# Performance work log

Measured on AMD Instinct MI355X. Metric: run time of the kernel, lower is better.

Reference implementation:

```python
import jax, jax.numpy as jnp
import numpy as np

FEATURE_DIM = 128
HIDDEN_DIM = 64
MAPPING_SIZE = 64
SCALE = 10.0
B, N, H, W = 8, 65536, 56, 56


def setup_inputs() -> dict:
    key = jax.random.key(0)
    ks = jax.random.split(key, 12)
    features = jax.random.normal(ks[0], (B, FEATURE_DIM, H, W), dtype=jnp.float32)
    # points in [-1, 1]^3
    points = jax.random.uniform(ks[1], (B, N, 3), dtype=jnp.float32, minval=-1.0, maxval=1.0)
    # realistic pinhole intrinsics for a 56x56 feature map
    k_mat = jnp.array([[56.0, 0.0, 28.0], [0.0, 56.0, 28.0], [0.0, 0.0, 1.0]], dtype=jnp.float32)
    k = jnp.broadcast_to(k_mat, (B, 3, 3))
    # extrinsics: identity rotation, translate z by 2 so points are in front of camera
    rt_mat = jnp.concatenate([jnp.eye(3, dtype=jnp.float32), jnp.array([[0.0], [0.0], [2.0]], dtype=jnp.float32)], axis=1)
    rt = jnp.broadcast_to(rt_mat, (B, 3, 4))
    # learned params
    B_gauss = jax.random.normal(ks[2], (MAPPING_SIZE, 3), dtype=jnp.float32) * SCALE
    input_dim = FEATURE_DIM + 2 * MAPPING_SIZE
    W1 = jax.random.normal(ks[3], (input_dim, HIDDEN_DIM), dtype=jnp.float32) * 0.05
    b1 = jnp.zeros((HIDDEN_DIM,), dtype=jnp.float32)
    W2 = jax.random.normal(ks[4], (HIDDEN_DIM, HIDDEN_DIM), dtype=jnp.float32) * 0.05
    b2 = jnp.zeros((HIDDEN_DIM,), dtype=jnp.float32)
    W3 = jax.random.normal(ks[5], (HIDDEN_DIM, HIDDEN_DIM), dtype=jnp.float32) * 0.05
    b3 = jnp.zeros((HIDDEN_DIM,), dtype=jnp.float32)
    W4 = jax.random.normal(ks[6], (HIDDEN_DIM, 1), dtype=jnp.float32) * 0.05
    b4 = jnp.zeros((1,), dtype=jnp.float32)
    return {"features": features, "points": points, "k": k, "rt": rt,
            "B_gauss": B_gauss, "W1": W1, "b1": b1, "W2": W2, "b2": b2,
            "W3": W3, "b3": b3, "W4": W4, "b4": b4}


def _grid_sample_bilinear_zeros(grid, x, y):
    # grid: (B, C, H, W); x, y: (B, N) pixel coords (align_corners=False already unnormalized)
    Bc, C, Hc, Wc = grid.shape
    g = jnp.transpose(grid, (0, 2, 3, 1))  # (B, H, W, C)
    x0 = jnp.floor(x)
    y0 = jnp.floor(y)
    wx1 = x - x0  # frac
    wy1 = y - y0
    wx0 = 1.0 - wx1
    wy0 = 1.0 - wy1
    x0i = x0.astype(jnp.int32)
    y0i = y0.astype(jnp.int32)
    bidx = jnp.arange(Bc, dtype=jnp.int32)[:, None]  # (B, 1)

    def gather(ix, iy):
        inb = ((ix >= 0) & (ix < Wc) & (iy >= 0) & (iy < Hc)).astype(grid.dtype)  # (B, N)
        vals = g[bidx, jnp.clip(iy, 0, Hc - 1), jnp.clip(ix, 0, Wc - 1)]  # (B, N, C)
        return vals * inb[..., None]

    out = (gather(x0i, y0i) * (wx0 * wy0)[..., None]
           + gather(x0i + 1, y0i) * (wx1 * wy0)[..., None]
           + gather(x0i, y0i + 1) * (wx0 * wy1)[..., None]
           + gather(x0i + 1, y0i + 1) * (wx1 * wy1)[..., None])
    return out  # (B, N, C)


def reference(features, points, k, rt, B_gauss, W1, b1, W2, b2, W3, b3, W4, b4):
    Bc, Nc, _ = points.shape
    Hc, Wc = features.shape[-2:]
    # --- camera projection ---
    homo = jnp.concatenate([points, jnp.ones((Bc, Nc, 1), dtype=points.dtype)], axis=2)  # (B,N,4)
    cam = jnp.einsum('bij,bnj->bni', rt, homo)   # (B,N,3)
    img = jnp.einsum('bij,bnj->bni', k, cam)     # (B,N,3)
    z = img[:, :, 2:3] + 1e-8
    uv = img[:, :, :2] / z
    valid = (img[:, :, 2:3] > 0).astype(points.dtype)  # (B,N,1)
    u_norm = (2.0 * uv[..., 0] + 1.0) / Wc - 1.0
    v_norm = (2.0 * uv[..., 1] + 1.0) / Hc - 1.0
    # grid_sample align_corners=False unnormalization: ix = ((g+1)*W - 1)/2
    x = ((u_norm + 1.0) * Wc - 1.0) * 0.5
    y = ((v_norm + 1.0) * Hc - 1.0) * 0.5
    img_feats = _grid_sample_bilinear_zeros(features, x, y) * valid  # (B,N,C)
    # --- Fourier mapping ---
    x_proj = (2.0 * np.pi) * jnp.einsum('bnd,md->bnm', points, B_gauss)  # (B,N,M)
    coord_feats = jnp.concatenate([jnp.sin(x_proj), jnp.cos(x_proj)], axis=-1)  # (B,N,2M)
    # --- MLP ---
    inp = jnp.concatenate([img_feats, coord_feats], axis=2)  # (B,N,C+2M)
    h = jax.nn.relu(inp @ W1 + b1)
    h = jax.nn.relu(h @ W2 + b2)
    h = jax.nn.relu(h @ W3 + b3)
    out = h @ W4 + b4  # (B,N,1)
    return out
```

## Files before the change

kernel.cpp:

```cpp
#include <hip/hip_runtime.h>

#define FDIM 128
#define HDIM 64
#define MSIZE 64
#define IMG_W 56
#define IMG_H 56
#define NPIX (IMG_W * IMG_H)
#define NB 8
#define NPTS 65536

typedef _Float16 f16x8 __attribute__((ext_vector_type(8)));
typedef __fp16 hf16x2 __attribute__((ext_vector_type(2)));
typedef float f32x4 __attribute__((ext_vector_type(4)));

#define W2_OFF 16384
#define W3_OFF 20480
#define BG_OFF 49152
#define FT_BYTE_OFF 50176
#define TR16_BLOCKS (NPIX / 16 * NB)

__device__ __forceinline__ void lds_fence() {
    __asm__ volatile("s_waitcnt lgkmcnt(0)" ::: "memory");
}

__global__ __launch_bounds__(256) void prep_kernel(const float* __restrict__ in,
                                                   const float* __restrict__ W1,
                                                   const float* __restrict__ W2,
                                                   const float* __restrict__ W3,
                                                   const float* __restrict__ Bg,
                                                   _Float16* __restrict__ ws) {
    if (blockIdx.x < TR16_BLOCKS) {
        __shared__ float tile[16][133];
        _Float16* out = ws + FT_BYTE_OFF / 2;
        const int b = blockIdx.x / (NPIX / 16);
        const int pbase = (blockIdx.x % (NPIX / 16)) * 16;
        const int t = threadIdx.x;
        const float* src = in + (size_t)b * FDIM * NPIX;
        _Float16*    dst = out + (size_t)b * NPIX * FDIM;
        const int pq = t & 3;
        const int ch = t >> 2;
#pragma unroll
        for (int it = 0; it < 2; ++it) {
            const int c = it * 64 + ch;
            const float4 v = *(const float4*)(src + (size_t)c * NPIX + pbase + pq * 4);
            tile[pq * 4 + 0][c] = v.x;
            tile[pq * 4 + 1][c] = v.y;
            tile[pq * 4 + 2][c] = v.z;
            tile[pq * 4 + 3][c] = v.w;
        }
        __syncthreads();
        const int px = t >> 4;
        const int hk = (t & 15) * 8;
        union { f16x8 v; hf16x2 h[4]; } hv;
#pragma unroll
        for (int j = 0; j < 4; ++j)
            hv.h[j] = __builtin_amdgcn_cvt_pkrtz(tile[px][hk + 2 * j], tile[px][hk + 2 * j + 1]);
        *(f16x8*)(dst + (size_t)(pbase + px) * FDIM + hk) = hv.v;
    } else if (blockIdx.x < TR16_BLOCKS + 12) {
        const int t = (blockIdx.x - TR16_BLOCKS) * 256 + threadIdx.x;
        const int l = t & 63;
        const int q = l >> 4;
        const int col = l & 15;
        const int frag = t >> 6;
        if (frag < 32) {
            const int kt = frag >> 2, nt = frag & 3;
#pragma unroll
            for (int j = 0; j < 8; ++j) {
                int k = kt * 32 + q * 8 + j;
                int row = (k < 128) ? k : (128 + (k & 1) * 64 + ((k - 128) >> 1));
                ws[((size_t)(frag * 64 + l)) * 8 + j] = (_Float16)W1[row * HDIM + nt * 16 + col];
            }
        } else if (frag < 40) {
            const int f2 = frag - 32;
            const int kt = f2 >> 2, nt = f2 & 3;
#pragma unroll
            for (int j = 0; j < 8; ++j) {
                int row = kt * 32 + q * 8 + j;
                ws[W2_OFF + ((size_t)(f2 * 64 + l)) * 8 + j] = (_Float16)W2[row * HDIM + nt * 16 + col];
            }
        } else {
            const int f3 = frag - 40;
            const int kt = f3 >> 2, nt = f3 & 3;
#pragma unroll
            for (int j = 0; j < 8; ++j) {
                int row = kt * 32 + q * 8 + j;
                ws[W3_OFF + ((size_t)(f3 * 64 + l)) * 8 + j] = (_Float16)W3[row * HDIM + nt * 16 + col];
            }
        }
    } else {
        const int t = threadIdx.x;
        if (t < MSIZE) {
            float* bgs = (float*)((char*)ws + BG_OFF);
            bgs[t]       = Bg[t * 3 + 0];
            bgs[64 + t]  = Bg[t * 3 + 1];
            bgs[128 + t] = Bg[t * 3 + 2];
        }
    }
}

__global__ __launch_bounds__(256, 3) void decoder_mfma5(
    const _Float16* __restrict__ ft,
    const float* __restrict__ points,
    const float* __restrict__ Kmat, const float* __restrict__ Rt,
    const _Float16* __restrict__ wfrag,
    const float* __restrict__ b1, const float* __restrict__ b2,
    const float* __restrict__ b3,
    const float* __restrict__ W4, const float* __restrict__ b4,
    float* __restrict__ out) {
    __shared__ _Float16 w1l[16384];
    __shared__ _Float16 lds[4 * 32 * 72];
    const int tid = threadIdx.x;
    const int wid = tid >> 6;
    const int l   = tid & 63;
    const int q   = l >> 4;
    const int col = l & 15;
    const int b    = blockIdx.x & 7;
    const int grp  = blockIdx.x >> 3;
    const int base = b * NPTS + grp * 128 + wid * 32;
    _Float16* Ah = lds + wid * 32 * 72;
    const float* bgs = (const float*)((const char*)wfrag + BG_OFF);

#pragma unroll
    for (int i = 0; i < 8; ++i)
        ((f16x8*)w1l)[i * 256 + tid] = ((const f16x8*)wfrag)[i * 256 + tid];

    const int gid = base + (l & 31);
    const float px = points[(size_t)gid * 3 + 0];
    const float py = points[(size_t)gid * 3 + 1];
    const float pz = points[(size_t)gid * 3 + 2];
    const float* rt = Rt + b * 12;
    const float* km = Kmat + b * 9;
    float cx = rt[0] * px + rt[1] * py + rt[2]  * pz + rt[3];
    float cy = rt[4] * px + rt[5] * py + rt[6]  * pz + rt[7];
    float cz = rt[8] * px + rt[9] * py + rt[10] * pz + rt[11];
    float ix = km[0] * cx + km[1] * cy + km[2] * cz;
    float iy = km[3] * cx + km[4] * cy + km[5] * cz;
    float iz = km[6] * cx + km[7] * cy + km[8] * cz;
    float z  = iz + 1e-8f;
    float u  = ix / z;
    float v  = iy / z;
    float valid = (iz > 0.0f) ? 1.0f : 0.0f;
    float u_norm = (2.0f * u + 1.0f) / (float)IMG_W - 1.0f;
    float v_norm = (2.0f * v + 1.0f) / (float)IMG_H - 1.0f;
    float x = ((u_norm + 1.0f) * (float)IMG_W - 1.0f) * 0.5f;
    float y = ((v_norm + 1.0f) * (float)IMG_H - 1.0f) * 0.5f;
    float x0f = floorf(x), y0f = floorf(y);
    float wx1 = x - x0f, wy1 = y - y0f;
    float wx0 = 1.0f - wx1, wy0 = 1.0f - wy1;
    int x0 = (int)x0f, y0 = (int)y0f;
    int x1 = x0 + 1, y1 = y0 + 1;
    int x0c = x0 < 0 ? 0 : (x0 > IMG_W - 1 ? IMG_W - 1 : x0);
    int x1c = x1 < 0 ? 0 : (x1 > IMG_W - 1 ? IMG_W - 1 : x1);
    int y0c = y0 < 0 ? 0 : (y0 > IMG_H - 1 ? IMG_H - 1 : y0);
    int y1c = y1 < 0 ? 0 : (y1 > IMG_H - 1 ? IMG_H - 1 : y1);
    float mx0 = (x0 >= 0 && x0 < IMG_W) ? 1.0f : 0.0f;
    float mx1 = (x1 >= 0 && x1 < IMG_W) ? 1.0f : 0.0f;
    float my0 = (y0 >= 0 && y0 < IMG_H) ? 1.0f : 0.0f;
    float my1 = (y1 >= 0 && y1 < IMG_H) ? 1.0f : 0.0f;
    const int pb = b * NPIX;
    float r_w00 = wx0 * wy0 * mx0 * my0 * valid;
    float r_w10 = wx1 * wy0 * mx1 * my0 * valid;
    float r_w01 = wx0 * wy1 * mx0 * my1 * valid;
    float r_w11 = wx1 * wy1 * mx1 * my1 * valid;
    int r_i00 = (pb + y0c * IMG_W + x0c) * FDIM;
    int r_i10 = (pb + y0c * IMG_W + x1c) * FDIM;
    int r_i01 = (pb + y1c * IMG_W + x0c) * FDIM;
    int r_i11 = (pb + y1c * IMG_W + x1c) * FDIM;

    float wv0[2], wv1[2], wv2[2], wv3[2];
    int   iv0[2], iv1[2], iv2[2], iv3[2];
    float qx[2], qy[2], qz[2];
#pragma unroll
    for (int mt = 0; mt < 2; ++mt) {
        const int src = mt * 16 + col;
        wv0[mt] = __shfl(r_w00, src);
        wv1[mt] = __shfl(r_w10, src);
        wv2[mt] = __shfl(r_w01, src);
        wv3[mt] = __shfl(r_w11, src);
        iv0[mt] = __shfl(r_i00, src);
        iv1[mt] = __shfl(r_i10, src);
        iv2[mt] = __shfl(r_i01, src);
        iv3[mt] = __shfl(r_i11, src);
        qx[mt]  = __shfl(px, src);
        qy[mt]  = __shfl(py, src);
        qz[mt]  = __shfl(pz, src);
    }

    __syncthreads();

    const f32x4 zero4 = {0.0f, 0.0f, 0.0f, 0.0f};
    f32x4 acc[2][4];
#pragma unroll
    for (int mt = 0; mt < 2; ++mt)
#pragma unroll
        for (int nt = 0; nt < 4; ++nt) acc[mt][nt] = zero4;

    const int co0 = q * 8;
    f16x8 a00 = *(const f16x8*)(ft + iv0[0] + co0);
    f16x8 a10 = *(const f16x8*)(ft + iv1[0] + co0);
    f16x8 a01 = *(const f16x8*)(ft + iv2[0] + co0);
    f16x8 a11 = *(const f16x8*)(ft + iv3[0] + co0);
    const int co1 = 32 + q * 8;
    f16x8 e00 = *(const f16x8*)(ft + iv0[0] + co1);
    f16x8 e10 = *(const f16x8*)(ft + iv1[0] + co1);
    f16x8 e01 = *(const f16x8*)(ft + iv2[0] + co1);
    f16x8 e11 = *(const f16x8*)(ft + iv3[0] + co1);

#pragma unroll
    for (int ktf = 0; ktf < 4; ++ktf) {
        const f32x4 bgx = *(const f32x4*)(bgs + ktf * 16 + q * 4);
        const f32x4 bgy = *(const f32x4*)(bgs + 64 + ktf * 16 + q * 4);
        const f32x4 bgz = *(const f32x4*)(bgs + 128 + ktf * 16 + q * 4);
        f16x8 bf[4];
#pragma unroll
        for (int nt = 0; nt < 4; ++nt)
            bf[nt] = *(const f16x8*)(w1l + ((size_t)(((4 + ktf) * 4 + nt) * 64 + l)) * 8);
#pragma unroll
        for (int mt = 0; mt < 2; ++mt) {
            union { f16x8 v; hf16x2 h[4]; } af;
#pragma unroll
            for (int i = 0; i < 4; ++i) {
                float t = bgx[i] * qx[mt] + bgy[i] * qy[mt] + bgz[i] * qz[mt];
                float tf = __builtin_amdgcn_fractf(t);
                af.h[i] = __builtin_amdgcn_cvt_pkrtz(__builtin_amdgcn_sinf(tf),
                                                     __builtin_amdgcn_cosf(tf));
            }
#pragma unroll
            for (int nt = 0; nt < 4; ++nt)
                acc[mt][nt] = __builtin_amdgcn_mfma_f32_16x16x32_f16(af.v, bf[nt], acc[mt][nt], 0, 0, 0);
        }
    }

    _Float16 wh[2][4];
#pragma unroll
    for (int mt = 0; mt < 2; ++mt) {
        wh[mt][0] = (_Float16)wv0[mt]; wh[mt][1] = (_Float16)wv1[mt];
        wh[mt][2] = (_Float16)wv2[mt]; wh[mt][3] = (_Float16)wv3[mt];
    }
#pragma unroll
    for (int s = 0; s < 8; ++s) {
        const int mt = s >> 2;
        f16x8 t00, t10, t01, t11;
        if (s < 6) {
            const int nmt = (s + 2) >> 2, nktg = (s + 2) & 3;
            const int co = nktg * 32 + q * 8;
            t00 = *(const f16x8*)(ft + iv0[nmt] + co);
            t10 = *(const f16x8*)(ft + iv1[nmt] + co);
            t01 = *(const f16x8*)(ft + iv2[nmt] + co);
            t11 = *(const f16x8*)(ft + iv3[nmt] + co);
        }
        f16x8 af = a00 * wh[mt][0] + a10 * wh[mt][1] + a01 * wh[mt][2] + a11 * wh[mt][3];
        const int ktg = s & 3;
#pragma unroll
        for (int nt = 0; nt < 4; ++nt) {
            f16x8 bf = *(const f16x8*)(w1l + ((size_t)((ktg * 4 + nt) * 64 + l)) * 8);
            acc[mt][nt] = __builtin_amdgcn_mfma_f32_16x16x32_f16(af, bf, acc[mt][nt], 0, 0, 0);
        }
        a00 = e00; a10 = e10; a01 = e01; a11 = e11;
        e00 = t00; e10 = t10; e01 = t01; e11 = t11;
    }

    f16x8 bfW[8];
#pragma unroll
    for (int f = 0; f < 8; ++f)
        bfW[f] = *(const f16x8*)(wfrag + W2_OFF + ((size_t)(f * 64 + l)) * 8);

    float bb[4];
#pragma unroll
    for (int nt = 0; nt < 4; ++nt) bb[nt] = b1[nt * 16 + col];
#pragma unroll
    for (int mt = 0; mt < 2; ++mt)
#pragma unroll
        for (int nt = 0; nt < 4; ++nt)
#pragma unroll
            for (int r = 0; r < 4; ++r) {
                float hv = fmaxf(acc[mt][nt][r] + bb[nt], 0.0f);
                Ah[(mt * 16 + q * 4 + r) * 72 + nt * 16 + col] = (_Float16)hv;
            }
    lds_fence();

#pragma unroll
    for (int mt = 0; mt < 2; ++mt)
#pragma unroll
        for (int nt = 0; nt < 4; ++nt) acc[mt][nt] = zero4;
#pragma unroll
    for (int ktl = 0; ktl < 2; ++ktl)
#pragma unroll
        for (int mt = 0; mt < 2; ++mt) {
            f16x8 af = *(const f16x8*)(&Ah[(mt * 16 + col) * 72 + ktl * 32 + q * 8]);
#pragma unroll
            for (int nt = 0; nt < 4; ++nt)
                acc[mt][nt] = __builtin_amdgcn_mfma_f32_16x16x32_f16(af, bfW[ktl * 4 + nt], acc[mt][nt], 0, 0, 0);
        }

#pragma unroll
    for (int f = 0; f < 8; ++f)
        bfW[f] = *(const f16x8*)(wfrag + W3_OFF + ((size_t)(f * 64 + l)) * 8);

    lds_fence();
#pragma unroll
    for (int nt = 0; nt < 4; ++nt) bb[nt] = b2[nt * 16 + col];
#pragma unroll
    for (int mt = 0; mt < 2; ++mt)
#pragma unroll
        for (int nt = 0; nt < 4; ++nt)
#pragma unroll
            for (int r = 0; r < 4; ++r) {
                float hv = fmaxf(acc[mt][nt][r] + bb[nt], 0.0f);
                Ah[(mt * 16 + q * 4 + r) * 72 + nt * 16 + col] = (_Float16)hv;
            }
    lds_fence();

#pragma unroll
    for (int mt = 0; mt < 2; ++mt)
#pragma unroll
        for (int nt = 0; nt < 4; ++nt) acc[mt][nt] = zero4;
#pragma unroll
    for (int ktl = 0; ktl < 2; ++ktl)
#pragma unroll
        for (int mt = 0; mt < 2; ++mt) {
            f16x8 af = *(const f16x8*)(&Ah[(mt * 16 + col) * 72 + ktl * 32 + q * 8]);
#pragma unroll
            for (int nt = 0; nt < 4; ++nt)
                acc[mt][nt] = __builtin_amdgcn_mfma_f32_16x16x32_f16(af, bfW[ktl * 4 + nt], acc[mt][nt], 0, 0, 0);
        }

    float b3v[4], w4v[4];
#pragma unroll
    for (int nt = 0; nt < 4; ++nt) {
        b3v[nt] = b3[nt * 16 + col];
        w4v[nt] = W4[nt * 16 + col];
    }
    const float b4v = b4[0];
#pragma unroll
    for (int mt = 0; mt < 2; ++mt)
#pragma unroll
        for (int r = 0; r < 4; ++r) {
            float p = 0.0f;
#pragma unroll
            for (int nt = 0; nt < 4; ++nt)
                p = fmaf(fmaxf(acc[mt][nt][r] + b3v[nt], 0.0f), w4v[nt], p);
            p += __shfl_xor(p, 1);
            p += __shfl_xor(p, 2);
            p += __shfl_xor(p, 4);
            p += __shfl_xor(p, 8);
            if (col == 0) out[base + mt * 16 + q * 4 + r] = p + b4v;
        }
}

__global__ __launch_bounds__(64, 2) void decoder_valu(
    const float* __restrict__ feats, const float* __restrict__ points,
    const float* __restrict__ Kmat, const float* __restrict__ Rt,
    const float* __restrict__ Bg,
    const float* __restrict__ W1, const float* __restrict__ b1,
    const float* __restrict__ W2, const float* __restrict__ b2,
    const float* __restrict__ W3, const float* __restrict__ b3,
    const float* __restrict__ W4, const float* __restrict__ b4,
    float* __restrict__ out) {
    __shared__ float hbuf[64 * 65];
    const int tid = threadIdx.x;
    const int b   = blockIdx.x / (NPTS / 64);
    const int gid = blockIdx.x * 64 + tid;
    const float px = points[(size_t)gid * 3 + 0];
    const float py = points[(size_t)gid * 3 + 1];
    const float pz = points[(size_t)gid * 3 + 2];
    const float* rt = Rt + b * 12;
    const float* km = Kmat + b * 9;
    float cx = rt[0] * px + rt[1] * py + rt[2]  * pz + rt[3];
    float cy = rt[4] * px + rt[5] * py + rt[6]  * pz + rt[7];
    float cz = rt[8] * px + rt[9] * py + rt[10] * pz + rt[11];
    float ix = km[0] * cx + km[1] * cy + km[2] * cz;
    float iy = km[3] * cx + km[4] * cy + km[5] * cz;
    float iz = km[6] * cx + km[7] * cy + km[8] * cz;
    float z  = iz + 1e-8f;
    float u  = ix / z, v = iy / z;
    float valid = (iz > 0.0f) ? 1.0f : 0.0f;
    float u_norm = (2.0f * u + 1.0f) / (float)IMG_W - 1.0f;
    float v_norm = (2.0f * v + 1.0f) / (float)IMG_H - 1.0f;
    float x = ((u_norm + 1.0f) * (float)IMG_W - 1.0f) * 0.5f;
    float y = ((v_norm + 1.0f) * (float)IMG_H - 1.0f) * 0.5f;
    float x0f = floorf(x), y0f = floorf(y);
    float wx1 = x - x0f, wy1 = y - y0f;
    float wx0 = 1.0f - wx1, wy0 = 1.0f - wy1;
    int x0 = (int)x0f, y0 = (int)y0f;
    int x1 = x0 + 1, y1 = y0 + 1;
    int x0c = x0 < 0 ? 0 : (x0 > IMG_W - 1 ? IMG_W - 1 : x0);
    int x1c = x1 < 0 ? 0 : (x1 > IMG_W - 1 ? IMG_W - 1 : x1);
    int y0c = y0 < 0 ? 0 : (y0 > IMG_H - 1 ? IMG_H - 1 : y0);
    int y1c = y1 < 0 ? 0 : (y1 > IMG_H - 1 ? IMG_H - 1 : y1);
    float mx0 = (x0 >= 0 && x0 < IMG_W) ? 1.0f : 0.0f;
    float mx1 = (x1 >= 0 && x1 < IMG_W) ? 1.0f : 0.0f;
    float my0 = (y0 >= 0 && y0 < IMG_H) ? 1.0f : 0.0f;
    float my1 = (y1 >= 0 && y1 < IMG_H) ? 1.0f : 0.0f;
    float w00 = wx0 * wy0 * mx0 * my0 * valid;
    float w10 = wx1 * wy0 * mx1 * my0 * valid;
    float w01 = wx0 * wy1 * mx0 * my1 * valid;
    float w11 = wx1 * wy1 * mx1 * my1 * valid;
    float h[HDIM];
#pragma unroll
    for (int j = 0; j < HDIM; ++j) h[j] = b1[j];
    const float* fb = feats + (size_t)b * FDIM * NPIX;
    const int p00 = y0c * IMG_W + x0c, p10 = y0c * IMG_W + x1c;
    const int p01 = y1c * IMG_W + x0c, p11 = y1c * IMG_W + x1c;
#pragma unroll 1
    for (int c = 0; c < FDIM; ++c) {
        const float* fp = fb + (size_t)c * NPIX;
        float fv = w00 * fp[p00] + w10 * fp[p10] + w01 * fp[p01] + w11 * fp[p11];
        const float* wr = W1 + (size_t)c * HDIM;
#pragma unroll
        for (int j = 0; j < HDIM; ++j) h[j] = fmaf(fv, wr[j], h[j]);
    }
#pragma unroll 1
    for (int m = 0; m < MSIZE; ++m) {
        float t = Bg[m * 3 + 0] * px + Bg[m * 3 + 1] * py + Bg[m * 3 + 2] * pz;
        float tf = t - floorf(t);
        float s = __builtin_amdgcn_sinf(tf);
        float c = __builtin_amdgcn_cosf(tf);
        const float* wsn = W1 + (size_t)(FDIM + m) * HDIM;
        const float* wcs = W1 + (size_t)(FDIM + MSIZE + m) * HDIM;
#pragma unroll
        for (int j = 0; j < HDIM; ++j)
            h[j] = fmaf(s, wsn[j], fmaf(c, wcs[j], h[j]));
    }
    float* myh = &hbuf[tid * 65];
#pragma unroll
    for (int j = 0; j < HDIM; ++j) myh[j] = fmaxf(h[j], 0.0f);
    float h2[HDIM];
#pragma unroll
    for (int j = 0; j < HDIM; ++j) h2[j] = b2[j];
#pragma unroll 1
    for (int i = 0; i < HDIM; ++i) {
        float hi = myh[i];
        const float* wr = W2 + (size_t)i * HDIM;
#pragma unroll
        for (int j = 0; j < HDIM; ++j) h2[j] = fmaf(hi, wr[j], h2[j]);
    }
#pragma unroll
    for (int j = 0; j < HDIM; ++j) myh[j] = fmaxf(h2[j], 0.0f);
#pragma unroll
    for (int j = 0; j < HDIM; ++j) h[j] = b3[j];
#pragma unroll 1
    for (int i = 0; i < HDIM; ++i) {
        float hi = myh[i];
        const float* wr = W3 + (size_t)i * HDIM;
#pragma unroll
        for (int j = 0; j < HDIM; ++j) h[j] = fmaf(hi, wr[j], h[j]);
    }
    float acc = b4[0];
#pragma unroll
    for (int j = 0; j < HDIM; ++j) acc = fmaf(fmaxf(h[j], 0.0f), W4[j], acc);
    out[gid] = acc;
}

extern "C" void kernel_launch(void* const* d_in, const int* in_sizes, int n_in,
                              void* d_out, int out_size, void* d_ws, size_t ws_size,
                              hipStream_t stream) {
    const float* feats = (const float*)d_in[0];
    const float* pts   = (const float*)d_in[1];
    const float* k     = (const float*)d_in[2];
    const float* rt    = (const float*)d_in[3];
    const float* Bg    = (const float*)d_in[4];
    const float* W1    = (const float*)d_in[5];
    const float* b1    = (const float*)d_in[6];
    const float* W2    = (const float*)d_in[7];
    const float* b2    = (const float*)d_in[8];
    const float* W3    = (const float*)d_in[9];
    const float* b3    = (const float*)d_in[10];
    const float* W4    = (const float*)d_in[11];
    const float* b4    = (const float*)d_in[12];
    float* out = (float*)d_out;

    const size_t ftBytes = (size_t)NB * NPIX * FDIM * sizeof(_Float16);

    if (ws_size >= FT_BYTE_OFF + ftBytes) {
        _Float16* wf = (_Float16*)d_ws;
        _Float16* ft = (_Float16*)((char*)d_ws + FT_BYTE_OFF);
        prep_kernel<<<TR16_BLOCKS + 13, 256, 0, stream>>>(feats, W1, W2, W3, Bg, wf);
        decoder_mfma5<<<NB * NPTS / 128, 256, 0, stream>>>(ft, pts, k, rt, wf,
                                                           b1, b2, b3, W4, b4, out);
    } else {
        decoder_valu<<<NB * NPTS / 64, 64, 0, stream>>>(feats, pts, k, rt, Bg,
                                                        W1, b1, W2, b2, W3, b3, W4, b4, out);
    }
}
```

Baseline: 174.0 us.

## Process two 32-point tiles per wave and prefetch second tile's gathers during MLP tail

Each wave now handles 64 points, split into two 32-point tiles that run one after the other, and the grid shrinks to half as many blocks. All 64 lanes now do the projection math, where before only 32 lanes did useful work. The second tile's feature gathers are issued before the first tile's MLP tail runs, so their latency can overlap that compute. It also halves how often each block copies W1 into LDS. The risks are higher register pressure from the second prefetch set, and fewer blocks for latency hiding.

Result: slower. 181.6 us (+4.4%).

```diff
diff --git a/kernel.cpp b/kernel.cpp
--- a/kernel.cpp
+++ b/kernel.cpp
@@ -98,7 +98,194 @@
     }
 }
 
-__global__ __launch_bounds__(256, 3) void decoder_mfma5(
+struct Rec {
+    float w0[2], w1[2], w2[2], w3[2];
+    int   i0[2], i1[2], i2[2], i3[2];
+    float qx[2], qy[2], qz[2];
+};
+struct Pref {
+    f16x8 a00, a10, a01, a11;
+    f16x8 e00, e10, e01, e11;
+};
+
+__device__ __forceinline__ Pref pre_issue(const _Float16* __restrict__ ft,
+                                          const Rec& R, int q) {
+    Pref P;
+    const int co0 = q * 8;
+    P.a00 = *(const f16x8*)(ft + R.i0[0] + co0);
+    P.a10 = *(const f16x8*)(ft + R.i1[0] + co0);
+    P.a01 = *(const f16x8*)(ft + R.i2[0] + co0);
+    P.a11 = *(const f16x8*)(ft + R.i3[0] + co0);
+    const int co1 = 32 + q * 8;
+    P.e00 = *(const f16x8*)(ft + R.i0[0] + co1);
+    P.e10 = *(const f16x8*)(ft + R.i1[0] + co1);
+    P.e01 = *(const f16x8*)(ft + R.i2[0] + co1);
+    P.e11 = *(const f16x8*)(ft + R.i3[0] + co1);
+    return P;
+}
+
+__device__ __forceinline__ void phaseF(f32x4 acc[2][4], const _Float16* __restrict__ w1l,
+                                       const float* __restrict__ bgs, const Rec& R,
+                                       int q, int l) {
+#pragma unroll
+    for (int ktf = 0; ktf < 4; ++ktf) {
+        const f32x4 bgx = *(const f32x4*)(bgs + ktf * 16 + q * 4);
+        const f32x4 bgy = *(const f32x4*)(bgs + 64 + ktf * 16 + q * 4);
+        const f32x4 bgz = *(const f32x4*)(bgs + 128 + ktf * 16 + q * 4);
+        f16x8 bf[4];
+#pragma unroll
+        for (int nt = 0; nt < 4; ++nt)
+            bf[nt] = *(const f16x8*)(w1l + ((size_t)(((4 + ktf) * 4 + nt) * 64 + l)) * 8);
+#pragma unroll
+        for (int mt = 0; mt < 2; ++mt) {
+            union { f16x8 v; hf16x2 h[4]; } af;
+#pragma unroll
+            for (int i = 0; i < 4; ++i) {
+                float t = bgx[i] * R.qx[mt] + bgy[i] * R.qy[mt] + bgz[i] * R.qz[mt];
+                float tf = __builtin_amdgcn_fractf(t);
+                af.h[i] = __builtin_amdgcn_cvt_pkrtz(__builtin_amdgcn_sinf(tf),
+                                                     __builtin_amdgcn_cosf(tf));
+            }
+#pragma unroll
+            for (int nt = 0; nt < 4; ++nt)
+                acc[mt][nt] = __builtin_amdgcn_mfma_f32_16x16x32_f16(af.v, bf[nt], acc[mt][nt], 0, 0, 0);
+        }
+    }
+}
+
+__device__ __forceinline__ void phaseI(f32x4 acc[2][4], const _Float16* __restrict__ ft,
+                                       const _Float16* __restrict__ w1l, const Rec& R,
+                                       Pref& P, int q, int l) {
+    _Float16 wh[2][4];
+#pragma unroll
+    for (int mt = 0; mt < 2; ++mt) {
+        wh[mt][0] = (_Float16)R.w0[mt]; wh[mt][1] = (_Float16)R.w1[mt];
+        wh[mt][2] = (_Float16)R.w2[mt]; wh[mt][3] = (_Float16)R.w3[mt];
+    }
+#pragma unroll
+    for (int s = 0; s < 8; ++s) {
+        const int mt = s >> 2;
+        f16x8 t00, t10, t01, t11;
+        if (s < 6) {
+            const int nmt = (s + 2) >> 2, nktg = (s + 2) & 3;
+            const int co = nktg * 32 + q * 8;
+            t00 = *(const f16x8*)(ft + R.i0[nmt] + co);
+            t10 = *(const f16x8*)(ft + R.i1[nmt] + co);
+            t01 = *(const f16x8*)(ft + R.i2[nmt] + co);
+            t11 = *(const f16x8*)(ft + R.i3[nmt] + co);
+        }
+        f16x8 af = P.a00 * wh[mt][0] + P.a10 * wh[mt][1] + P.a01 * wh[mt][2] + P.a11 * wh[mt][3];
+        const int ktg = s & 3;
+#pragma unroll
+        for (int nt = 0; nt < 4; ++nt) {
+            f16x8 bf = *(const f16x8*)(w1l + ((size_t)((ktg * 4 + nt) * 64 + l)) * 8);
+            acc[mt][nt] = __builtin_amdgcn_mfma_f32_16x16x32_f16(af, bf, acc[mt][nt], 0, 0, 0);
+        }
+        P.a00 = P.e00; P.a10 = P.e10; P.a01 = P.e01; P.a11 = P.e11;
+        P.e00 = t00; P.e10 = t10; P.e01 = t01; P.e11 = t11;
+    }
+}
+
+__device__ __forceinline__ void mlp_tail(f32x4 acc[2][4], _Float16* __restrict__ Ah,
+                                         const _Float16* __restrict__ wfrag,
+                                         const float* __restrict__ b1,
+                                         const float* __restrict__ b2,
+                                         const float* __restrict__ b3,
+                                         const float* __restrict__ W4,
+                                         const float* __restrict__ b4,
+                                         float* __restrict__ out, int outbase,
+                                         int q, int col, int l) {
+    const f32x4 zero4 = {0.0f, 0.0f, 0.0f, 0.0f};
+    f16x8 bfW[8];
+#pragma unroll
+    for (int f = 0; f < 8; ++f)
+        bfW[f] = *(const f16x8*)(wfrag + W2_OFF + ((size_t)(f * 64 + l)) * 8);
+
+    float bb[4];
+#pragma unroll
+    for (int nt = 0; nt < 4; ++nt) bb[nt] = b1[nt * 16 + col];
+#pragma unroll
+    for (int mt = 0; mt < 2; ++mt)
+#pragma unroll
+        for (int nt = 0; nt < 4; ++nt)
+#pragma unroll
+            for (int r = 0; r < 4; ++r) {
+                float hv = fmaxf(acc[mt][nt][r] + bb[nt], 0.0f);
+                Ah[(mt * 16 + q * 4 + r) * 72 + nt * 16 + col] = (_Float16)hv;
+            }
+    lds_fence();
+
+#pragma unroll
+    for (int mt = 0; mt < 2; ++mt)
+#pragma unroll
+        for (int nt = 0; nt < 4; ++nt) acc[mt][nt] = zero4;
+#pragma unroll
+    for (int ktl = 0; ktl < 2; ++ktl)
+#pragma unroll
+        for (int mt = 0; mt < 2; ++mt) {
+            f16x8 af = *(const f16x8*)(&Ah[(mt * 16 + col) * 72 + ktl * 32 + q * 8]);
+#pragma unroll
+            for (int nt = 0; nt < 4; ++nt)
+                acc[mt][nt] = __builtin_amdgcn_mfma_f32_16x16x32_f16(af, bfW[ktl * 4 + nt], acc[mt][nt], 0, 0, 0);
+        }
+
+#pragma unroll
+    for (int f = 0; f < 8; ++f)
+        bfW[f] = *(const f16x8*)(wfrag + W3_OFF + ((size_t)(f * 64 + l)) * 8);
+
+    lds_fence();
+#pragma unroll
+    for (int nt = 0; nt < 4; ++nt) bb[nt] = b2[nt * 16 + col];
+#pragma unroll
+    for (int mt = 0; mt < 2; ++mt)
+#pragma unroll
+        for (int nt = 0; nt < 4; ++nt)
+#pragma unroll
+            for (int r = 0; r < 4; ++r) {
+                float hv = fmaxf(acc[mt][nt][r] + bb[nt], 0.0f);
+                Ah[(mt * 16 + q * 4 + r) * 72 + nt * 16 + col] = (_Float16)hv;
+            }
+    lds_fence();
+
+#pragma unroll
+    for (int mt = 0; mt < 2; ++mt)
+#pragma unroll
+        for (int nt = 0; nt < 4; ++nt) acc[mt][nt] = zero4;
+#pragma unroll
+    for (int ktl = 0; ktl < 2; ++ktl)
+#pragma unroll
+        for (int mt = 0; mt < 2; ++mt) {
+            f16x8 af = *(const f16x8*)(&Ah[(mt * 16 + col) * 72 + ktl * 32 + q * 8]);
+#pragma unroll
+            for (int nt = 0; nt < 4; ++nt)
+                acc[mt][nt] = __builtin_amdgcn_mfma_f32_16x16x32_f16(af, bfW[ktl * 4 + nt], acc[mt][nt], 0, 0, 0);
+        }
+
+    float b3v[4], w4v[4];
+#pragma unroll
+    for (int nt = 0; nt < 4; ++nt) {
+        b3v[nt] = b3[nt * 16 + col];
+        w4v[nt] = W4[nt * 16 + col];
+    }
+    const float b4v = b4[0];
+#pragma unroll
+    for (int mt = 0; mt < 2; ++mt)
+#pragma unroll
+        for (int r = 0; r < 4; ++r) {
+            float p = 0.0f;
+#pragma unroll
+            for (int nt = 0; nt < 4; ++nt)
+                p = fmaf(fmaxf(acc[mt][nt][r] + b3v[nt], 0.0f), w4v[nt], p);
+            p += __shfl_xor(p, 1);
+            p += __shfl_xor(p, 2);
+            p += __shfl_xor(p, 4);
+            p += __shfl_xor(p, 8);
+            if (col == 0) out[outbase + mt * 16 + q * 4 + r] = p + b4v;
+        }
+    lds_fence();
+}
+
+__global__ __launch_bounds__(256, 3) void decoder_mfma6(
     const _Float16* __restrict__ ft,
     const float* __restrict__ points,
     const float* __restrict__ Kmat, const float* __restrict__ Rt,
@@ -114,9 +301,9 @@
     const int l   = tid & 63;
     const int q   = l >> 4;
     const int col = l & 15;
-    const int b    = blockIdx.x & 7;
-    const int grp  = blockIdx.x >> 3;
-    const int base = b * NPTS + grp * 128 + wid * 32;
+    const int b     = blockIdx.x & 7;
+    const int grp   = blockIdx.x >> 3;
+    const int wbase = b * NPTS + grp * 256 + wid * 64;
     _Float16* Ah = lds + wid * 32 * 72;
     const float* bgs = (const float*)((const char*)wfrag + BG_OFF);
 
@@ -124,7 +311,7 @@
     for (int i = 0; i < 8; ++i)
         ((f16x8*)w1l)[i * 256 + tid] = ((const f16x8*)wfrag)[i * 256 + tid];
 
-    const int gid = base + (l & 31);
+    const int gid = wbase + l;
     const float px = points[(size_t)gid * 3 + 0];
     const float py = points[(size_t)gid * 3 + 1];
     const float pz = points[(size_t)gid * 3 + 2];
@@ -167,185 +354,63 @@
     int r_i01 = (pb + y1c * IMG_W + x0c) * FDIM;
     int r_i11 = (pb + y1c * IMG_W + x1c) * FDIM;
 
-    float wv0[2], wv1[2], wv2[2], wv3[2];
-    int   iv0[2], iv1[2], iv2[2], iv3[2];
-    float qx[2], qy[2], qz[2];
+    Rec R0;
 #pragma unroll
     for (int mt = 0; mt < 2; ++mt) {
         const int src = mt * 16 + col;
-        wv0[mt] = __shfl(r_w00, src);
-        wv1[mt] = __shfl(r_w10, src);
-        wv2[mt] = __shfl(r_w01, src);
-        wv3[mt] = __shfl(r_w11, src);
-        iv0[mt] = __shfl(r_i00, src);
-        iv1[mt] = __shfl(r_i10, src);
-        iv2[mt] = __shfl(r_i01, src);
-        iv3[mt] = __shfl(r_i11, src);
-        qx[mt]  = __shfl(px, src);
-        qy[mt]  = __shfl(py, src);
-        qz[mt]  = __shfl(pz, src);
-    }
+        R0.w0[mt] = __shfl(r_w00, src);
+        R0.w1[mt] = __shfl(r_w10, src);
+        R0.w2[mt] = __shfl(r_w01, src);
+        R0.w3[mt] = __shfl(r_w11, src);
+        R0.i0[mt] = __shfl(r_i00, src);
+        R0.i1[mt] = __shfl(r_i10, src);
+        R0.i2[mt] = __shfl(r_i01, src);
+        R0.i3[mt] = __shfl(r_i11, src);
+        R0.qx[mt] = __shfl(px, src);
+        R0.qy[mt] = __shfl(py, src);
+        R0.qz[mt] = __shfl(pz, src);
+    }
+    Pref P0 = pre_issue(ft, R0, q);
 
     __syncthreads();
 
+    f32x4 acc[2][4];
     const f32x4 zero4 = {0.0f, 0.0f, 0.0f, 0.0f};
-    f32x4 acc[2][4];
 #pragma unroll
     for (int mt = 0; mt < 2; ++mt)
 #pragma unroll
         for (int nt = 0; nt < 4; ++nt) acc[mt][nt] = zero4;
 
-    const int co0 = q * 8;
-    f16x8 a00 = *(const f16x8*)(ft + iv0[0] + co0);
-    f16x8 a10 = *(const f16x8*)(ft + iv1[0] + co0);
-    f16x8 a01 = *(const f16x8*)(ft + iv2[0] + co0);
-    f16x8 a11 = *(const f16x8*)(ft + iv3[0] + co0);
-    const int co1 = 32 + q * 8;
-    f16x8 e00 = *(const f16x8*)(ft + iv0[0] + co1);
-    f16x8 e10 = *(const f16x8*)(ft + iv1[0] + co1);
-    f16x8 e01 = *(const f16x8*)(ft + iv2[0] + co1);
-    f16x8 e11 = *(const f16x8*)(ft + iv3[0] + co1);
-
-#pragma unroll
-    for (int ktf = 0; ktf < 4; ++ktf) {
-        const f32x4 bgx = *(const f32x4*)(bgs + ktf * 16 + q * 4);
-        const f32x4 bgy = *(const f32x4*)(bgs + 64 + ktf * 16 + q * 4);
-        const f32x4 bgz = *(const f32x4*)(bgs + 128 + ktf * 16 + q * 4);
-        f16x8 bf[4];
-#pragma unroll
-        for (int nt = 0; nt < 4; ++nt)
-            bf[nt] = *(const f16x8*)(w1l + ((size_t)(((4 + ktf) * 4 + nt) * 64 + l)) * 8);
-#pragma unroll
-        for (int mt = 0; mt < 2; ++mt) {
-            union { f16x8 v; hf16x2 h[4]; } af;
-#pragma unroll
-            for (int i = 0; i < 4; ++i) {
-                float t = bgx[i] * qx[mt] + bgy[i] * qy[mt] + bgz[i] * qz[mt];
-                float tf = __builtin_amdgcn_fractf(t);
-                af.h[i] = __builtin_amdgcn_cvt_pkrtz(__builtin_amdgcn_sinf(tf),
-                                                     __builtin_amdgcn_cosf(tf));
-            }
-#pragma unroll
-            for (int nt = 0; nt < 4; ++nt)
-                acc[mt][nt] = __builtin_amdgcn_mfma_f32_16x16x32_f16(af.v, bf[nt], acc[mt][nt], 0, 0, 0);
-        }
-    }
-
-    _Float16 wh[2][4];
+    phaseF(acc, w1l, bgs, R0, q, l);
+    phaseI(acc, ft, w1l, R0, P0, q, l);
+
+    Rec R1;
 #pragma unroll
     for (int mt = 0; mt < 2; ++mt) {
-        wh[mt][0] = (_Float16)wv0[mt]; wh[mt][1] = (_Float16)wv1[mt];
-        wh[mt][2] = (_Float16)wv2[mt]; wh[mt][3] = (_Float16)wv3[mt];
-    }
-#pragma unroll
-    for (int s = 0; s < 8; ++s) {
-        const int mt = s >> 2;
-        f16x8 t00, t10, t01, t11;
-        if (s < 6) {
-            const int nmt = (s + 2) >> 2, nktg = (s + 2) & 3;
-            const int co = nktg * 32 + q * 8;
-            t00 = *(const f16x8*)(ft + iv0[nmt] + co);
-            t10 = *(const f16x8*)(ft + iv1[nmt] + co);
-            t01 = *(const f16x8*)(ft + iv2[nmt] + co);
-            t11 = *(const f16x8*)(ft + iv3[nmt] + co);
-        }
-        f16x8 af = a00 * wh[mt][0] + a10 * wh[mt][1] + a01 * wh[mt][2] + a11 * wh[mt][3];
-        const int ktg = s & 3;
-#pragma unroll
-        for (int nt = 0; nt < 4; ++nt) {
-            f16x8 bf = *(const f16x8*)(w1l + ((size_t)((ktg * 4 + nt) * 64 + l)) * 8);
-            acc[mt][nt] = __builtin_amdgcn_mfma_f32_16x16x32_f16(af, bf, acc[mt][nt], 0, 0, 0);
-        }
-        a00 = e00; a10 = e10; a01 = e01; a11 = e11;
-        e00 = t00; e10 = t10; e01 = t01; e11 = t11;
-    }
-
-    f16x8 bfW[8];
-#pragma unroll
-    for (int f = 0; f < 8; ++f)
-        bfW[f] = *(const f16x8*)(wfrag + W2_OFF + ((size_t)(f * 64 + l)) * 8);
-
-    float bb[4];
-#pragma unroll
-    for (int nt = 0; nt < 4; ++nt) bb[nt] = b1[nt * 16 + col];
-#pragma unroll
-    for (int mt = 0; mt < 2; ++mt)
-#pragma unroll
-        for (int nt = 0; nt < 4; ++nt)
-#pragma unroll
-            for (int r = 0; r < 4; ++r) {
-                float hv = fmaxf(acc[mt][nt][r] + bb[nt], 0.0f);
-                Ah[(mt * 16 + q * 4 + r) * 72 + nt * 16 + col] = (_Float16)hv;
-            }
-    lds_fence();
+        const int src = 32 + mt * 16 + col;
+        R1.w0[mt] = __shfl(r_w00, src);
+        R1.w1[mt] = __shfl(r_w10, src);
+        R1.w2[mt] = __shfl(r_w01, src);
+        R1.w3[mt] = __shfl(r_w11, src);
+        R1.i0[mt] = __shfl(r_i00, src);
+        R1.i1[mt] = __shfl(r_i10, src);
+        R1.i2[mt] = __shfl(r_i01, src);
+        R1.i3[mt] = __shfl(r_i11, src);
+        R1.qx[mt] = __shfl(px, src);
+        R1.qy[mt] = __shfl(py, src);
+        R1.qz[mt] = __shfl(pz, src);
+    }
+    Pref P1 = pre_issue(ft, R1, q);
+
+    mlp_tail(acc, Ah, wfrag, b1, b2, b3, W4, b4, out, wbase, q, col, l);
 
 #pragma unroll
     for (int mt = 0; mt < 2; ++mt)
 #pragma unroll
         for (int nt = 0; nt < 4; ++nt) acc[mt][nt] = zero4;
-#pragma unroll
-    for (int ktl = 0; ktl < 2; ++ktl)
-#pragma unroll
-        for (int mt = 0; mt < 2; ++mt) {
-            f16x8 af = *(const f16x8*)(&Ah[(mt * 16 + col) * 72 + ktl * 32 + q * 8]);
-#pragma unroll
-            for (int nt = 0; nt < 4; ++nt)
-                acc[mt][nt] = __builtin_amdgcn_mfma_f32_16x16x32_f16(af, bfW[ktl * 4 + nt], acc[mt][nt], 0, 0, 0);
-        }
-
-#pragma unroll
-    for (int f = 0; f < 8; ++f)
-        bfW[f] = *(const f16x8*)(wfrag + W3_OFF + ((size_t)(f * 64 + l)) * 8);
-
-    lds_fence();
-#pragma unroll
-    for (int nt = 0; nt < 4; ++nt) bb[nt] = b2[nt * 16 + col];
-#pragma unroll
-    for (int mt = 0; mt < 2; ++mt)
-#pragma unroll
-        for (int nt = 0; nt < 4; ++nt)
-#pragma unroll
-            for (int r = 0; r < 4; ++r) {
-                float hv = fmaxf(acc[mt][nt][r] + bb[nt], 0.0f);
-                Ah[(mt * 16 + q * 4 + r) * 72 + nt * 16 + col] = (_Float16)hv;
-            }
-    lds_fence();
-
-#pragma unroll
-    for (int mt = 0; mt < 2; ++mt)
-#pragma unroll
-        for (int nt = 0; nt < 4; ++nt) acc[mt][nt] = zero4;
-#pragma unroll
-    for (int ktl = 0; ktl < 2; ++ktl)
-#pragma unroll
-        for (int mt = 0; mt < 2; ++mt) {
-            f16x8 af = *(const f16x8*)(&Ah[(mt * 16 + col) * 72 + ktl * 32 + q * 8]);
-#pragma unroll
-            for (int nt = 0; nt < 4; ++nt)
-                acc[mt][nt] = __builtin_amdgcn_mfma_f32_16x16x32_f16(af, bfW[ktl * 4 + nt], acc[mt][nt], 0, 0, 0);
-        }
-
-    float b3v[4], w4v[4];
-#pragma unroll
-    for (int nt = 0; nt < 4; ++nt) {
-        b3v[nt] = b3[nt * 16 + col];
-        w4v[nt] = W4[nt * 16 + col];
-    }
-    const float b4v = b4[0];
-#pragma unroll
-    for (int mt = 0; mt < 2; ++mt)
-#pragma unroll
-        for (int r = 0; r < 4; ++r) {
-            float p = 0.0f;
-#pragma unroll
-            for (int nt = 0; nt < 4; ++nt)
-                p = fmaf(fmaxf(acc[mt][nt][r] + b3v[nt], 0.0f), w4v[nt], p);
-            p += __shfl_xor(p, 1);
-            p += __shfl_xor(p, 2);
-            p += __shfl_xor(p, 4);
-            p += __shfl_xor(p, 8);
-            if (col == 0) out[base + mt * 16 + q * 4 + r] = p + b4v;
-        }
+    phaseF(acc, w1l, bgs, R1, q, l);
+    phaseI(acc, ft, w1l, R1, P1, q, l);
+    mlp_tail(acc, Ah, wfrag, b1, b2, b3, W4, b4, out, wbase + 32, q, col, l);
 }
 
 __global__ __launch_bounds__(64, 2) void decoder_valu(
@@ -476,7 +541,7 @@
         _Float16* wf = (_Float16*)d_ws;
         _Float16* ft = (_Float16*)((char*)d_ws + FT_BYTE_OFF);
         prep_kernel<<<TR16_BLOCKS + 13, 256, 0, stream>>>(feats, W1, W2, W3, Bg, wf);
-        decoder_mfma5<<<NB * NPTS / 128, 256, 0, stream>>>(ft, pts, k, rt, wf,
+        decoder_mfma6<<<NB * NPTS / 256, 256, 0, stream>>>(ft, pts, k, rt, wf,
                                                            b1, b2, b3, W4, b4, out);
     } else {
         decoder_valu<<<NB * NPTS / 64, 64, 0, stream>>>(feats, pts, k, rt, Bg,
```
